# Optimization experiments

Hardware: AMD Instinct MI355X
Metric: run time of the kernel (lower is better)

The kernel has to match this reference:

```python
import jax, jax.numpy as jnp
import numpy as np

B, L, D, H = 2, 2048, 1024, 16
HD = D // H


def setup_inputs() -> dict:
    key = jax.random.key(0)
    ks = jax.random.split(key, 12)
    s = 1.0 / np.sqrt(D)
    inp = {
        "q": jax.random.normal(ks[0], (B, L, D), jnp.float32),
        "k": jax.random.normal(ks[1], (B, L, D), jnp.float32),
        "v": jax.random.normal(ks[2], (B, L, D), jnp.float32),
        "mask": jnp.zeros((B, L), dtype=bool),  # True = masked out
        "Wq": jax.random.normal(ks[3], (D, D), jnp.float32) * s,
        "bq": jnp.zeros((D,), jnp.float32),
        "Wk": jax.random.normal(ks[4], (D, D), jnp.float32) * s,
        "bk": jnp.zeros((D,), jnp.float32),
        "Wv": jax.random.normal(ks[5], (D, D), jnp.float32) * s,
        "bv": jnp.zeros((D,), jnp.float32),
        "Wo": jax.random.normal(ks[6], (D, D), jnp.float32) * s,
        "bo": jnp.zeros((D,), jnp.float32),
    }
    return inp


def reference(q, k, v, mask, Wq, bq, Wk, bk, Wv, bv, Wo, bo):
    # linear projections (torch Linear: x @ W.T + b), split into heads: [B,H,L,HD]
    def proj(x, W, b):
        y = jnp.einsum('bld,ed->ble', x, W) + b
        return y.reshape(x.shape[0], x.shape[1], H, HD).transpose(0, 2, 1, 3)

    Q = proj(q, Wq, bq)
    K = proj(k, Wk, bk)
    V = proj(v, Wv, bv)

    scale = 1.0 / np.sqrt(HD).astype(np.float32)
    scores = jnp.einsum('bhqd,bhkd->bhqk', Q, K) * scale  # [B,H,Lq,Lk]
    # mask [B,Lk] -> broadcast over heads and query positions
    scores = jnp.where(mask[:, None, None, :], -jnp.inf, scores)
    attn = jax.nn.softmax(scores, axis=-1)
    out = jnp.einsum('bhqk,bhkd->bhqd', attn, V)  # [B,H,Lq,HD]
    out = out.transpose(0, 2, 1, 3).reshape(q.shape[0], q.shape[1], D)
    return jnp.einsum('bld,ed->ble', out, Wo) + bo
```

## Files before the change

### kernel.cpp

```cpp
#include <hip/hip_runtime.h>

#define LSEQ 2048
#define DMODEL 1024
#define NHEAD 16
#define HDIM 64

typedef __attribute__((ext_vector_type(8))) short bf16x8;
typedef __attribute__((ext_vector_type(4))) float f32x4;
typedef __attribute__((ext_vector_type(16))) float f32x16;
typedef unsigned int u32;
typedef unsigned short u16;
typedef unsigned long long u64;

static __device__ __forceinline__ u16 f2bf(float x) {
    return (u16)((__builtin_bit_cast(u32, x) + 0x8000u) >> 16);
}

static __device__ __forceinline__ u32 f2bf_pk(float hi, float lo) {
    u32 a = __builtin_bit_cast(u32, hi) + 0x8000u;
    u32 b = __builtin_bit_cast(u32, lo) + 0x8000u;
#if __has_builtin(__builtin_amdgcn_perm)
    return __builtin_amdgcn_perm(a, b, 0x07060302u);
#else
    return (a & 0xFFFF0000u) | (b >> 16);
#endif
}

static __device__ __forceinline__ float bf2f(short s) {
    return __builtin_bit_cast(float, (u32)((u16)s) << 16);
}

static __device__ __forceinline__ float fast_exp2(float x) {
#if __has_builtin(__builtin_amdgcn_exp2f)
    return __builtin_amdgcn_exp2f(x);
#else
    return __expf(x * 0.6931471805599453f);
#endif
}

static __device__ __forceinline__ void gll16(const void* g, void* l) {
    __builtin_amdgcn_global_load_lds(
        (const __attribute__((address_space(1))) u32*)g,
        (__attribute__((address_space(3))) u32*)l, 16, 0, 0);
}

template <int N>
static __device__ __forceinline__ void vwait() {
    asm volatile("s_waitcnt vmcnt(%0)" :: "n"(N) : "memory");
}

__global__ __launch_bounds__(256) void conv_all(
    const float* __restrict__ q, const float* __restrict__ k, const float* __restrict__ v,
    const float* __restrict__ w0, const float* __restrict__ w1,
    const float* __restrict__ w2, const float* __restrict__ w3,
    u16* __restrict__ Qf, u16* __restrict__ Kf, u16* __restrict__ Vf,
    u16* __restrict__ o0, u16* __restrict__ o1, u16* __restrict__ o2,
    u16* __restrict__ o3) {
    const int bid = blockIdx.x;
    const float* s; u16* d; int off;
    if (bid < 12288) {
        const int z = bid >> 12;
        off = bid & 4095;
        if (z == 0)      { s = q; d = Qf; }
        else if (z == 1) { s = k; d = Kf; }
        else             { s = v; d = Vf; }
    } else {
        const int t = bid - 12288;
        const int z = t >> 10;
        off = t & 1023;
        if (z == 0)      { s = w0; d = o0; }
        else if (z == 1) { s = w1; d = o1; }
        else if (z == 2) { s = w2; d = o2; }
        else             { s = w3; d = o3; }
    }
    const int i = (off * 256 + threadIdx.x) * 4;
    float4 x = *(const float4*)(s + i);
    uint2 r;
    r.x = f2bf_pk(x.y, x.x);
    r.y = f2bf_pk(x.w, x.z);
    *(uint2*)(d + i) = r;
}

template <int OUT_MODE, int BN>
__device__ __forceinline__ void mfma_gemm(u16* __restrict__ sm,
                                          const u16* __restrict__ Xb,
                                          const u16* __restrict__ Wb,
                                          const float* __restrict__ bias,
                                          void* __restrict__ Yv, float scale) {
    constexpr int NB = BN / 32;
    constexpr int LPT = (BN == 128) ? 4 : 3;
    constexpr int ASZ = 4096;
    constexpr int BSZ = BN * 32;
    constexpr int NT = DMODEL / 32;
    u16* As = sm;
    u16* Bs = sm + 3 * ASZ;

    const int tid = threadIdx.x;
    const int wave = tid >> 6, lane = tid & 63;
    const int l16 = lane & 15, quad = lane >> 4;
    const int wm = (wave >> 1) * 64, wn = (wave & 1) * (BN / 2);
    const int m0 = blockIdx.x * 128, n0 = blockIdx.y * BN;

    const u16* Xr = Xb + (size_t)(m0 + (tid >> 2)) * DMODEL + (tid & 3) * 8;
    const u16* Wr = Wb + (size_t)(n0 + (tid >> 2)) * DMODEL + (tid & 3) * 8;
    const int t8 = tid * 8;

    auto stage = [&](int kt, int slot) {
        const int k0 = kt * 32;
        u16* Ab = As + slot * ASZ;
        u16* Bb = Bs + slot * BSZ;
        gll16(Xr + k0, Ab + t8);
        gll16(Xr + (size_t)64 * DMODEL + k0, Ab + 2048 + t8);
        gll16(Wr + k0, Bb + t8);
        if (BN == 128)
            gll16(Wr + (size_t)64 * DMODEL + k0, Bb + 2048 + t8);
    };

    f32x4 acc[4][NB];
    #pragma unroll
    for (int i = 0; i < 4; ++i)
        #pragma unroll
        for (int j = 0; j < NB; ++j)
            #pragma unroll
            for (int r = 0; r < 4; ++r) acc[i][j][r] = 0.0f;

    auto compute = [&](int kt) {
        const u16* Ac = As + (kt % 3) * ASZ;
        const u16* Bc = Bs + (kt % 3) * BSZ;
        bf16x8 af[4], bf[NB];
        #pragma unroll
        for (int mb = 0; mb < 4; ++mb)
            af[mb] = *(const bf16x8*)(Ac + (wm + mb * 16 + l16) * 32 + quad * 8);
        #pragma unroll
        for (int nb = 0; nb < NB; ++nb)
            bf[nb] = *(const bf16x8*)(Bc + (wn + nb * 16 + l16) * 32 + quad * 8);
        #pragma unroll
        for (int mb = 0; mb < 4; ++mb)
            #pragma unroll
            for (int nb = 0; nb < NB; ++nb)
                acc[mb][nb] = __builtin_amdgcn_mfma_f32_16x16x32_bf16(
                    af[mb], bf[nb], acc[mb][nb], 0, 0, 0);
    };

    stage(0, 0);
    stage(1, 1);

    #pragma unroll 1
    for (int kt = 0; kt < NT - 1; ++kt) {
        vwait<LPT>();
        __builtin_amdgcn_s_barrier();
        if (kt + 2 < NT) stage(kt + 2, (kt + 2) % 3);
        compute(kt);
    }
    vwait<0>();
    __builtin_amdgcn_s_barrier();
    compute(NT - 1);

    #pragma unroll
    for (int nb = 0; nb < NB; ++nb) {
        const int n = n0 + wn + nb * 16 + l16;
        const float bn = bias[n];
        #pragma unroll
        for (int mb = 0; mb < 4; ++mb) {
            const int mb0 = m0 + wm + mb * 16 + quad * 4;
            if (OUT_MODE == 2) {
                u16* Y = (u16*)Yv;
                uint2 rr;
                rr.x = f2bf_pk((acc[mb][nb][1] + bn) * scale, (acc[mb][nb][0] + bn) * scale);
                rr.y = f2bf_pk((acc[mb][nb][3] + bn) * scale, (acc[mb][nb][2] + bn) * scale);
                const int bb = mb0 >> 11, l = mb0 & 2047;
                const int h = n >> 6, hd = n & 63;
                *(uint2*)(Y + ((size_t)((bb * NHEAD + h) * HDIM) + hd) * LSEQ + l) = rr;
            } else {
                #pragma unroll
                for (int r = 0; r < 4; ++r) {
                    const int m = mb0 + r;
                    const float val = (acc[mb][nb][r] + bn) * scale;
                    if (OUT_MODE == 0) {
                        u16* Y = (u16*)Yv;
                        const int bb = m >> 11, l = m & 2047;
                        const int h = n >> 6, hd = n & 63;
                        Y[(((size_t)(bb * NHEAD + h) * LSEQ + l) * HDIM) + hd] = f2bf(val);
                    } else {
                        float* Y = (float*)Yv;
                        Y[(size_t)m * DMODEL + n] = val;
                    }
                }
            }
        }
    }
}

#define QSCALE (0.125f * 1.4426950408889634f)

__global__ __launch_bounds__(256) void qkv_gemm(
    const u16* __restrict__ Qf, const u16* __restrict__ Kf, const u16* __restrict__ Vf,
    const u16* __restrict__ Wqb, const u16* __restrict__ Wkb, const u16* __restrict__ Wvb,
    const float* __restrict__ bq, const float* __restrict__ bk, const float* __restrict__ bv,
    u16* __restrict__ Qp, u16* __restrict__ Kp, u16* __restrict__ Vtp) {
    __shared__ alignas(16) u16 sm[24576];
    if (blockIdx.z == 0)      mfma_gemm<0, 128>(sm, Qf, Wqb, bq, (void*)Qp, QSCALE);
    else if (blockIdx.z == 1) mfma_gemm<0, 128>(sm, Kf, Wkb, bk, (void*)Kp, 1.0f);
    else                      mfma_gemm<2, 128>(sm, Vf, Wvb, bv, (void*)Vtp, 1.0f);
}

__global__ __launch_bounds__(256) void out_gemm(
    const u16* __restrict__ AOb, const u16* __restrict__ Wob,
    const float* __restrict__ bo, float* __restrict__ out) {
    __shared__ alignas(16) u16 sm[18432];
    mfma_gemm<1, 64>(sm, AOb, Wob, bo, (void*)out, 1.0f);
}

#define KT 128
#define NTILE (LSEQ / KT)
#define HTILE (NTILE / 2)

__global__ __launch_bounds__(512, 2) void attn_mfma(
    const u16* __restrict__ Qp, const u16* __restrict__ Kp,
    const u16* __restrict__ Vtp, const unsigned char* __restrict__ mask,
    u16* __restrict__ P0, u16* __restrict__ P1, float* __restrict__ lbuf) {
    __shared__ alignas(16) u16 smem[40960];

    const int tid = threadIdx.x;
    const int wave = tid >> 6;
    const int lane = tid & 63;
    const int l32 = lane & 31;
    const int half = lane >> 5;
    const int bh = blockIdx.x;
    const int b = bh >> 4;
    const int h = bh & 15;
    const int q0 = blockIdx.y * 256;
    const int qw = q0 + wave * 32;
    const int z = blockIdx.z;
    const int kt0 = z * HTILE, kt1 = kt0 + HTILE;

    u16* Pz = z ? P1 : P0;
    float* lb = lbuf + z * (32 * LSEQ);

    const u16* Qg = Qp + ((size_t)bh * LSEQ + qw) * HDIM;
    const u16* Kg = Kp + (size_t)bh * LSEQ * HDIM;
    const u16* Vtg = Vtp + (size_t)bh * HDIM * LSEQ;
    const unsigned char* mg = mask + (size_t)b * LSEQ;

    bf16x8 qf[4];
    #pragma unroll
    for (int dc = 0; dc < 4; ++dc)
        qf[dc] = *(const bf16x8*)(Qg + (size_t)l32 * HDIM + dc * 16 + half * 8);

    f32x16 o0 = {}, o1 = {};
    const f32x16 zc = {};
    float ls[4] = {0.0f, 0.0f, 0.0f, 0.0f};

    auto stageK = [&](int ktile, int slot) {
        const int k0 = ktile * KT;
        u16* Kb = smem + slot * 8192;
        #pragma unroll
        for (int j = 0; j < 2; ++j) {
            const int cid = j * 512 + tid;
            const int key = cid >> 3, pc = cid & 7, c = pc ^ (key & 7);
            gll16(Kg + (size_t)(k0 + key) * HDIM + c * 8, Kb + cid * 8);
        }
    };
    auto stageV = [&](int ktile, int slot) {
        const int k0 = ktile * KT;
        u16* Vb = smem + 16384 + slot * 8192;
        #pragma unroll
        for (int j = 0; j < 2; ++j) {
            const int cid = j * 512 + tid;
            const int d = cid >> 4, pc = cid & 15, c = pc ^ (d & 15);
            gll16(Vtg + (size_t)d * LSEQ + k0 + c * 8, Vb + cid * 8);
        }
    };

    stageK(kt0, kt0 & 1); stageV(kt0, kt0 % 3);

    const u64* mg8 = (const u64*)mg;
    const u64 mm = mg8[lane] | mg8[lane + 64] | mg8[lane + 128] | mg8[lane + 192];
    const bool mask_any = __any((int)(mm != 0ULL));

    __syncthreads();

    u32 pk[4][8];

    for (int kt = kt0; kt < kt1; ++kt) {
        if (kt + 1 < kt1) {
            stageK(kt + 1, (kt + 1) & 1);
            stageV(kt + 1, (kt + 1) % 3);
        }
        const u16* Kb = smem + (kt & 1) * 8192;

        f32x16 st[4];
        #pragma unroll
        for (int kb = 0; kb < 4; ++kb) {
            const int key = kb * 32 + l32;
            const int phys = half ^ (key & 7);
            bf16x8 kf = *(const bf16x8*)(Kb + key * 64 + phys * 8);
            st[kb] = __builtin_amdgcn_mfma_f32_32x32x16_bf16(kf, qf[0], zc, 0, 0, 0);
        }
        #pragma unroll
        for (int dc = 1; dc < 4; ++dc)
            #pragma unroll
            for (int kb = 0; kb < 4; ++kb) {
                const int key = kb * 32 + l32;
                const int phys = (dc * 2 + half) ^ (key & 7);
                bf16x8 kf = *(const bf16x8*)(Kb + key * 64 + phys * 8);
                st[kb] = __builtin_amdgcn_mfma_f32_32x32x16_bf16(kf, qf[dc], st[kb], 0, 0, 0);
            }

        if (kt > kt0) {
            const u16* Vbp = smem + 16384 + ((kt + 2) % 3) * 8192;
            #pragma unroll
            for (int c = 0; c < 8; ++c) {
                const int kb = c >> 1, wb = 4 * (c & 1);
                bf16x8 pb = __builtin_bit_cast(bf16x8, *(uint4*)&pk[kb][wb]);
                {
                    const int d = l32;
                    const int phys = (c * 2 + half) ^ (d & 15);
                    bf16x8 va = *(const bf16x8*)(Vbp + d * 128 + phys * 8);
                    o0 = __builtin_amdgcn_mfma_f32_32x32x16_bf16(va, pb, o0, 0, 0, 0);
                }
                {
                    const int d = 32 + l32;
                    const int phys = (c * 2 + half) ^ (d & 15);
                    bf16x8 va = *(const bf16x8*)(Vbp + d * 128 + phys * 8);
                    o1 = __builtin_amdgcn_mfma_f32_32x32x16_bf16(va, pb, o1, 0, 0, 0);
                }
            }
        }

        if (mask_any) {
            const int k0 = kt * KT;
            const int mb0 = mg[k0 + lane];
            const int mb1 = mg[k0 + 64 + lane];
            const float b0f = mb0 ? -1e30f : 0.0f;
            const float b1f = mb1 ? -1e30f : 0.0f;
            #pragma unroll
            for (int kb = 0; kb < 4; ++kb)
                #pragma unroll
                for (int r = 0; r < 16; ++r) {
                    const int key = kb * 32 + (r & 3) + 8 * (r >> 2) + 4 * half;
                    const float bv = __shfl((kb < 2) ? b0f : b1f, key & 63, 64);
                    st[kb][r] += bv;
                }
        }

        u32 pkn[4][8];
        #pragma unroll
        for (int kb = 0; kb < 4; ++kb)
            #pragma unroll
            for (int w = 0; w < 8; ++w) {
                const float plo = fast_exp2(st[kb][2 * w]);
                const float phi = fast_exp2(st[kb][2 * w + 1]);
                ls[kb] += plo + phi;
                pkn[kb][w] = f2bf_pk(phi, plo);
            }
        #pragma unroll
        for (int kb = 0; kb < 4; ++kb)
            #pragma unroll
            for (int wb = 0; wb < 8; wb += 4) {
#if __has_builtin(__builtin_amdgcn_permlane32_swap)
                auto r02 = __builtin_amdgcn_permlane32_swap(
                    (int)pkn[kb][wb],     (int)pkn[kb][wb + 2], false, false);
                auto r13 = __builtin_amdgcn_permlane32_swap(
                    (int)pkn[kb][wb + 1], (int)pkn[kb][wb + 3], false, false);
                pk[kb][wb]     = (u32)r02[0]; pk[kb][wb + 2] = (u32)r02[1];
                pk[kb][wb + 1] = (u32)r13[0]; pk[kb][wb + 3] = (u32)r13[1];
#else
                const u32 ta = half ? pkn[kb][wb] : pkn[kb][wb + 2];
                const u32 tb = half ? pkn[kb][wb + 1] : pkn[kb][wb + 3];
                const u32 xa = __shfl_xor((int)ta, 32, 64);
                const u32 xb = __shfl_xor((int)tb, 32, 64);
                pk[kb][wb]     = half ? xa : pkn[kb][wb];
                pk[kb][wb + 1] = half ? xb : pkn[kb][wb + 1];
                pk[kb][wb + 2] = half ? pkn[kb][wb + 2] : xa;
                pk[kb][wb + 3] = half ? pkn[kb][wb + 3] : xb;
#endif
            }

        __syncthreads();
    }

    {
        const u16* Vbp = smem + 16384 + ((kt1 - 1) % 3) * 8192;
        #pragma unroll
        for (int c = 0; c < 8; ++c) {
            const int kb = c >> 1, wb = 4 * (c & 1);
            bf16x8 pb = __builtin_bit_cast(bf16x8, *(uint4*)&pk[kb][wb]);
            {
                const int d = l32;
                const int phys = (c * 2 + half) ^ (d & 15);
                bf16x8 va = *(const bf16x8*)(Vbp + d * 128 + phys * 8);
                o0 = __builtin_amdgcn_mfma_f32_32x32x16_bf16(va, pb, o0, 0, 0, 0);
            }
            {
                const int d = 32 + l32;
                const int phys = (c * 2 + half) ^ (d & 15);
                bf16x8 va = *(const bf16x8*)(Vbp + d * 128 + phys * 8);
                o1 = __builtin_amdgcn_mfma_f32_32x32x16_bf16(va, pb, o1, 0, 0, 0);
            }
        }
    }

    const float l_l = (ls[0] + ls[1]) + (ls[2] + ls[3]);
    const float l_tot = l_l + __shfl_xor(l_l, 32, 64);
    if (!half) lb[bh * LSEQ + qw + l32] = l_tot;
    __syncthreads();
    u16* T = smem;
    #pragma unroll
    for (int nb = 0; nb < 2; ++nb)
        #pragma unroll
        for (int rp = 0; rp < 8; ++rp) {
            const int r = rp * 2;
            const int d = nb * 32 + (r & 3) + 8 * (r >> 2) + 4 * half;
            const float vlo = (nb ? o1[r] : o0[r]);
            const float vhi = (nb ? o1[r + 1] : o0[r + 1]);
            *(u32*)(T + (wave * 32 + l32) * 72 + d) = f2bf_pk(vhi, vlo);
        }
    __syncthreads();
    #pragma unroll
    for (int i = 0; i < 4; ++i) {
        const int cid = i * 512 + tid;
        const int row = cid >> 3, ch = cid & 7;
        bf16x8 val = *(const bf16x8*)(T + row * 72 + ch * 8);
        *(bf16x8*)(Pz + ((size_t)(b * LSEQ + q0 + row) * DMODEL) + h * HDIM + ch * 8) = val;
    }
}

__global__ __launch_bounds__(256) void combine(
    const u16* __restrict__ P0, const u16* __restrict__ P1,
    const float* __restrict__ lbuf, u16* __restrict__ AOb) {
    const int c = (blockIdx.x * 256 + threadIdx.x) * 8;
    const int bl = c >> 10;
    const int k = c & 1023;
    const int h = k >> 6;
    const int b = bl >> 11, l = bl & 2047;
    const int li = ((b << 4) + h) * LSEQ + l;
    const float inv = 1.0f / (lbuf[li] + lbuf[32 * LSEQ + li]);
    bf16x8 x0 = *(const bf16x8*)(P0 + c);
    bf16x8 x1 = *(const bf16x8*)(P1 + c);
    u32 r[4];
    #pragma unroll
    for (int j = 0; j < 4; ++j) {
        const float lo = (bf2f(x0[2 * j]) + bf2f(x1[2 * j])) * inv;
        const float hi = (bf2f(x0[2 * j + 1]) + bf2f(x1[2 * j + 1])) * inv;
        r[j] = f2bf_pk(hi, lo);
    }
    *(uint4*)(AOb + c) = *(uint4*)r;
}

extern "C" void kernel_launch(void* const* d_in, const int* in_sizes, int n_in,
                              void* d_out, int out_size, void* d_ws, size_t ws_size,
                              hipStream_t stream) {
    (void)in_sizes; (void)n_in; (void)out_size; (void)ws_size;
    const float* q  = (const float*)d_in[0];
    const float* k  = (const float*)d_in[1];
    const float* v  = (const float*)d_in[2];
    const unsigned char* mask = (const unsigned char*)d_in[3];
    const float* Wq = (const float*)d_in[4];
    const float* bq = (const float*)d_in[5];
    const float* Wk = (const float*)d_in[6];
    const float* bk = (const float*)d_in[7];
    const float* Wv = (const float*)d_in[8];
    const float* bv = (const float*)d_in[9];
    const float* Wo = (const float*)d_in[10];
    const float* bo = (const float*)d_in[11];
    float* out = (float*)d_out;

    u16* ws16 = (u16*)d_ws;
    const size_t M4 = (size_t)4 * 1024 * 1024;
    const size_t M1 = (size_t)1024 * 1024;
    u16* Qf  = ws16;
    u16* Kf  = ws16 + M4;
    u16* Vf  = ws16 + 2 * M4;
    u16* Qp  = ws16 + 3 * M4;
    u16* Kp  = ws16 + 4 * M4;
    u16* Vtp = ws16 + 5 * M4;
    u16* AOb = ws16 + 6 * M4;
    u16* Wqb = ws16 + 7 * M4;
    u16* Wkb = ws16 + 7 * M4 + M1;
    u16* Wvb = ws16 + 7 * M4 + 2 * M1;
    u16* Wob = ws16 + 7 * M4 + 3 * M1;

    u16* P0 = Qf;
    u16* P1 = Kf;
    float* lbuf = (float*)Vf;

    conv_all<<<dim3(16384), 256, 0, stream>>>(q, k, v, Wq, Wk, Wv, Wo,
                                              Qf, Kf, Vf, Wqb, Wkb, Wvb, Wob);
    qkv_gemm<<<dim3(32, 8, 3), 256, 0, stream>>>(Qf, Kf, Vf, Wqb, Wkb, Wvb,
                                                 bq, bk, bv, Qp, Kp, Vtp);
    attn_mfma<<<dim3(32, 8, 2), 512, 0, stream>>>(Qp, Kp, Vtp, mask, P0, P1, lbuf);
    combine<<<dim3(2048), 256, 0, stream>>>(P0, P1, lbuf, AOb);
    out_gemm<<<dim3(32, 16), 256, 0, stream>>>(AOb, Wob, bo, out);
}
```

Before: 218.6 us.

## Drop deferred PV software pipelining; do PV in same iteration with double-buffered V

```diff
diff --git a/kernel.cpp b/kernel.cpp
--- a/kernel.cpp
+++ b/kernel.cpp
@@ -219,7 +219,7 @@
     const u16* __restrict__ Qp, const u16* __restrict__ Kp,
     const u16* __restrict__ Vtp, const unsigned char* __restrict__ mask,
     u16* __restrict__ P0, u16* __restrict__ P1, float* __restrict__ lbuf) {
-    __shared__ alignas(16) u16 smem[40960];
+    __shared__ alignas(16) u16 smem[32768];
 
     const int tid = threadIdx.x;
     const int wave = tid >> 6;
@@ -272,7 +272,7 @@
         }
     };
 
-    stageK(kt0, kt0 & 1); stageV(kt0, kt0 % 3);
+    stageK(kt0, kt0 & 1); stageV(kt0, kt0 & 1);
 
     const u64* mg8 = (const u64*)mg;
     const u64 mm = mg8[lane] | mg8[lane + 64] | mg8[lane + 128] | mg8[lane + 192];
@@ -280,14 +280,13 @@
 
     __syncthreads();
 
-    u32 pk[4][8];
-
     for (int kt = kt0; kt < kt1; ++kt) {
         if (kt + 1 < kt1) {
             stageK(kt + 1, (kt + 1) & 1);
-            stageV(kt + 1, (kt + 1) % 3);
+            stageV(kt + 1, (kt + 1) & 1);
         }
         const u16* Kb = smem + (kt & 1) * 8192;
+        const u16* Vb = smem + 16384 + (kt & 1) * 8192;
 
         f32x16 st[4];
         #pragma unroll
@@ -306,27 +305,6 @@
                 bf16x8 kf = *(const bf16x8*)(Kb + key * 64 + phys * 8);
                 st[kb] = __builtin_amdgcn_mfma_f32_32x32x16_bf16(kf, qf[dc], st[kb], 0, 0, 0);
             }
-
-        if (kt > kt0) {
-            const u16* Vbp = smem + 16384 + ((kt + 2) % 3) * 8192;
-            #pragma unroll
-            for (int c = 0; c < 8; ++c) {
-                const int kb = c >> 1, wb = 4 * (c & 1);
-                bf16x8 pb = __builtin_bit_cast(bf16x8, *(uint4*)&pk[kb][wb]);
-                {
-                    const int d = l32;
-                    const int phys = (c * 2 + half) ^ (d & 15);
-                    bf16x8 va = *(const bf16x8*)(Vbp + d * 128 + phys * 8);
-                    o0 = __builtin_amdgcn_mfma_f32_32x32x16_bf16(va, pb, o0, 0, 0, 0);
-                }
-                {
-                    const int d = 32 + l32;
-                    const int phys = (c * 2 + half) ^ (d & 15);
-                    bf16x8 va = *(const bf16x8*)(Vbp + d * 128 + phys * 8);
-                    o1 = __builtin_amdgcn_mfma_f32_32x32x16_bf16(va, pb, o1, 0, 0, 0);
-                }
-            }
-        }
 
         if (mask_any) {
             const int k0 = kt * KT;
@@ -344,7 +322,7 @@
                 }
         }
 
-        u32 pkn[4][8];
+        u32 pkn[4][8], pk[4][8];
         #pragma unroll
         for (int kb = 0; kb < 4; ++kb)
             #pragma unroll
@@ -377,11 +355,6 @@
 #endif
             }
 
-        __syncthreads();
-    }
-
-    {
-        const u16* Vbp = smem + 16384 + ((kt1 - 1) % 3) * 8192;
         #pragma unroll
         for (int c = 0; c < 8; ++c) {
             const int kb = c >> 1, wb = 4 * (c & 1);
@@ -389,16 +362,18 @@
             {
                 const int d = l32;
                 const int phys = (c * 2 + half) ^ (d & 15);
-                bf16x8 va = *(const bf16x8*)(Vbp + d * 128 + phys * 8);
+                bf16x8 va = *(const bf16x8*)(Vb + d * 128 + phys * 8);
                 o0 = __builtin_amdgcn_mfma_f32_32x32x16_bf16(va, pb, o0, 0, 0, 0);
             }
             {
                 const int d = 32 + l32;
                 const int phys = (c * 2 + half) ^ (d & 15);
-                bf16x8 va = *(const bf16x8*)(Vbp + d * 128 + phys * 8);
+                bf16x8 va = *(const bf16x8*)(Vb + d * 128 + phys * 8);
                 o1 = __builtin_amdgcn_mfma_f32_32x32x16_bf16(va, pb, o1, 0, 0, 0);
             }
         }
+
+        __syncthreads();
     }
 
     const float l_l = (ls[0] + ls[1]) + (ls[2] + ls[3]);
```

Result: no change. 216.2 us (-1.1%).
